# Optimization experiments

Measured on AMD Instinct MI355X. Metric: run time of the kernel, lower is better.

The kernel has to match this reference:

```python
import jax, jax.numpy as jnp
import numpy as np

DIM = 256
B, W_IN, H_IN = 8, 96, 96


def setup_inputs() -> dict:
    key = jax.random.key(0)
    k1, k2, k3 = jax.random.split(key, 3)
    x = jax.random.normal(k1, (B, W_IN, H_IN, DIM), dtype=jnp.float32)
    # Conv2d(dim, 3*dim, kernel_size=1): weight (3C, C) (1x1 spatial dropped), bias (3C,)
    w_qkv = jax.random.normal(k2, (3 * DIM, DIM), dtype=jnp.float32) * (1.0 / np.sqrt(DIM))
    b_qkv = jax.random.normal(k3, (3 * DIM,), dtype=jnp.float32) * 0.01
    return {"x": x, "w_qkv": w_qkv, "b_qkv": b_qkv}


def reference(x, w_qkv, b_qkv):
    # x: (B, W, H, C) -> transpose(3,1) -> (B, C, H, W)
    xt = jnp.transpose(x, (0, 3, 2, 1))
    # 1x1 conv == channel GEMM
    qvk = jnp.einsum('bchw,oc->bohw', xt, w_qkv) + b_qkv[None, :, None, None]
    q, k, v = jnp.split(qvk, 3, axis=1)  # each (B, C, H, W)
    Bn, C, H, W = q.shape

    q_t = jnp.transpose(q, (0, 2, 1, 3))            # (B, H, C, W)
    qk = q_t.reshape(Bn, H * C, W)                   # (B, H*C, W)
    qf = q_t.reshape(Bn, H, C * W)                   # (B, H, C*W)
    kq = jnp.transpose(k, (0, 1, 3, 2)).reshape(Bn, C * W, H)  # (B, C*W, H)
    ms = jax.nn.softmax(jnp.matmul(qf, kq), axis=-1)  # (B, H, H) attention over H

    kf = jnp.transpose(k, (0, 3, 2, 1)).reshape(Bn, W, H * C)  # (B, W, H*C)
    ma = jax.nn.softmax(jnp.matmul(kf, qk), axis=-1)  # (B, W, W) attention over W

    vq = jnp.transpose(v, (0, 2, 1, 3)).reshape(Bn, H, C * W)  # (B, H, C*W)
    vk = jnp.transpose(v, (0, 3, 2, 1)).reshape(Bn, W, H * C)  # (B, W, H*C)

    ms = jnp.matmul(ms, vq).reshape(Bn, H, C, W)     # view(B, H, C, W)
    ms = jnp.transpose(ms, (0, 2, 1, 3))             # (B, C, H, W)
    ma = jnp.matmul(ma, vk).reshape(Bn, W, H, C)     # view(B, W, H, C)
    ma = jnp.transpose(ma, (0, 3, 2, 1))             # (B, C, H, W)

    # final transpose(3,1): (B, C, H, W) -> (B, W, H, C)
    return jnp.transpose(ms + ma, (0, 3, 2, 1))
```

## Files before the change

kernel.cpp:

```cpp
#include <hip/hip_runtime.h>
#include <math.h>

#define SQ 96
#define CQ 256
#define OQ 768
#define HWQ 9216
#define PIXQ 73728

typedef __attribute__((ext_vector_type(8))) __bf16 bf16x8;
typedef __attribute__((ext_vector_type(4))) float f32x4;

union FragU { uint4 u; bf16x8 b; };

__device__ inline uint32_t bf16_rne_u(float f) {
  uint32_t u = __float_as_uint(f);
  return (u + 0x7FFFu + ((u >> 16) & 1u)) >> 16;
}
__device__ inline uint32_t pack_split(float f) {
  uint32_t hi = bf16_rne_u(f);
  float rem = f - __uint_as_float(hi << 16);
  uint32_t lo = __float_as_uint(rem) >> 16;
  return hi | (lo << 16);
}

__device__ inline const uint32_t* swzc(const uint32_t* base, int row, int colb) {
  return base + row * 32 + ((colb ^ ((row & 7) << 4)) >> 2);
}

__device__ inline void lds_dma16(const void* g, void* l) {
  __builtin_amdgcn_global_load_lds(
      (const __attribute__((address_space(1))) uint32_t*)g,
      (__attribute__((address_space(3))) uint32_t*)l, 16, 0, 0);
}

__global__ __launch_bounds__(256) void split_tiles_kernel(
    const float* __restrict__ src, uint32_t* __restrict__ dst) {
  int t = blockIdx.x * 256 + threadIdx.x;
  int e = t * 8;
  int m = e >> 8;
  int rem = e & 255;
  int kc = rem >> 5;
  int k8 = (rem & 31) >> 3;
  const float* s = src + (size_t)m * 256 + rem;
  uint32_t h[4], l[4];
#pragma unroll
  for (int i = 0; i < 2; ++i) {
    float4 v = *(const float4*)(s + 4 * i);
    uint32_t p0 = pack_split(v.x), p1 = pack_split(v.y);
    uint32_t p2 = pack_split(v.z), p3 = pack_split(v.w);
    h[2 * i]     = (p0 & 0xFFFFu) | (p1 << 16);
    h[2 * i + 1] = (p2 & 0xFFFFu) | (p3 << 16);
    l[2 * i]     = (p0 >> 16) | (p1 & 0xFFFF0000u);
    l[2 * i + 1] = (p2 >> 16) | (p3 & 0xFFFF0000u);
  }
  int swz = (m & 7) << 4;
  uint32_t* rowp = dst + ((size_t)m * 8 + kc) * 32;
  *(uint4*)(rowp + (((k8 * 16) ^ swz) >> 2)) = *(uint4*)h;
  *(uint4*)(rowp + (((64 + k8 * 16) ^ swz) >> 2)) = *(uint4*)l;
}

__global__ __launch_bounds__(256) void qkv_gemm_mfma(
    const uint32_t* __restrict__ xps, const uint32_t* __restrict__ wps,
    const float* __restrict__ bias, ushort* __restrict__ qkh,
    ushort* __restrict__ qkl, ushort* __restrict__ vb) {
  __shared__ uint32_t Apk[128 * 32];
  __shared__ uint32_t Bpk[128 * 32];
  const int tid = threadIdx.x;
  const int lane = tid & 63;
  const int wid = tid >> 6;
  const int wm = wid >> 1, wn = wid & 1;
  const int lr = lane & 15, quad = lane >> 4;
  const int lin = (blockIdx.x & 7) * 432 + (blockIdx.x >> 3);
  const int m0 = (lin / 6) * 128, n0 = (lin % 6) * 128;
  const int srow = tid >> 3;
  const int scol = (tid & 7) * 4;

  f32x4 acc[4][4] = {};

  const uint32_t* aP = xps + (size_t)(m0 + srow) * 256 + scol;
  const uint32_t* bP = wps + (size_t)(n0 + srow) * 256 + scol;

  for (int kc = 0; kc < 8; ++kc) {
#pragma unroll
    for (int j = 0; j < 4; ++j) {
      lds_dma16(aP + j * 8192 + kc * 32, &Apk[j * 1024 + tid * 4]);
      lds_dma16(bP + j * 8192 + kc * 32, &Bpk[j * 1024 + tid * 4]);
    }
    __syncthreads();

    FragU ah[4], al[4], bh[4], bl[4];
#pragma unroll
    for (int t = 0; t < 4; ++t) {
      const int ra = wm * 64 + t * 16 + lr;
      ah[t].u = *(const uint4*)swzc(Apk, ra, quad * 16);
      al[t].u = *(const uint4*)swzc(Apk, ra, 64 + quad * 16);
      const int rb = wn * 64 + t * 16 + lr;
      bh[t].u = *(const uint4*)swzc(Bpk, rb, quad * 16);
      bl[t].u = *(const uint4*)swzc(Bpk, rb, 64 + quad * 16);
    }
#pragma unroll
    for (int i = 0; i < 4; ++i)
#pragma unroll
      for (int j = 0; j < 4; ++j) {
        acc[i][j] = __builtin_amdgcn_mfma_f32_16x16x32_bf16(al[i].b, bh[j].b, acc[i][j], 0, 0, 0);
        acc[i][j] = __builtin_amdgcn_mfma_f32_16x16x32_bf16(ah[i].b, bl[j].b, acc[i][j], 0, 0, 0);
        acc[i][j] = __builtin_amdgcn_mfma_f32_16x16x32_bf16(ah[i].b, bh[j].b, acc[i][j], 0, 0, 0);
      }
    __syncthreads();
  }

#pragma unroll
  for (int i = 0; i < 4; ++i) {
    const int growb = m0 + wm * 64 + i * 16 + quad * 4;
#pragma unroll
    for (int r = 0; r < 4; ++r) {
      int p = growb + r;
      int b = p / HWQ;
      int rem = p - b * HWQ;
      int ww = rem / SQ;
      int hh = rem - ww * SQ;
      size_t opix = (size_t)b * HWQ + (size_t)hh * SQ + ww;
#pragma unroll
      for (int j = 0; j < 4; ++j) {
        int o = n0 + wn * 64 + j * 16 + lr;
        float val = acc[i][j][r] + bias[o];
        if (o < 512) {
          uint32_t ps = pack_split(val);
          qkh[opix * 512 + o] = (ushort)ps;
          qkl[opix * 512 + o] = (ushort)(ps >> 16);
        } else {
          vb[opix * 256 + (o - 512)] = (ushort)bf16_rne_u(val);
        }
      }
    }
  }
}

__global__ __launch_bounds__(256) void attn_scores_mfma(
    const ushort* __restrict__ qkh, const ushort* __restrict__ qkl,
    float* __restrict__ Sh, float* __restrict__ Sw) {
  __shared__ uint32_t Xpk[96 * 32];
  __shared__ uint32_t Ypk[96 * 32];
  const int tid = threadIdx.x;
  const int lane = tid & 63;
  const int wid = tid >> 6;
  const int wm = wid >> 1, wn = wid & 1;
  const int lr = lane & 15, quad = lane >> 4;
  const int chunk = blockIdx.x;
  const int b = blockIdx.y;
  const int which = blockIdx.z;
  const size_t base = (size_t)b * HWQ * 512;
  const int offX = which ? 256 : 0;
  const int offY = which ? 0 : 256;
  const int srow = tid >> 3;
  const int byteoff = (tid & 7) * 16;

  f32x4 acc[3][3] = {};

  for (int it = 0; it < 24; ++it) {
    int kout = chunk * 3 + (it >> 3);
    int c0 = (it & 7) * 32;
#pragma unroll
    for (int j = 0; j < 3; ++j) {
      int row = j * 32 + srow;
      int nom = byteoff ^ ((row & 7) << 4);
      const ushort* plane = (nom & 64) ? qkl : qkh;
      int within = (nom & 63) >> 1;
      size_t pix = which ? ((size_t)kout * SQ + row) : ((size_t)row * SQ + kout);
      const ushort* sX = plane + base + pix * 512 + offX + c0 + within;
      const ushort* sY = plane + base + pix * 512 + offY + c0 + within;
      lds_dma16(sX, &Xpk[j * 1024 + tid * 4]);
      lds_dma16(sY, &Ypk[j * 1024 + tid * 4]);
    }
    __syncthreads();

    FragU xh[3], xl[3], yh[3], yl[3];
#pragma unroll
    for (int t = 0; t < 3; ++t) {
      const int rx = wm * 48 + t * 16 + lr;
      xh[t].u = *(const uint4*)swzc(Xpk, rx, quad * 16);
      xl[t].u = *(const uint4*)swzc(Xpk, rx, 64 + quad * 16);
      const int ry = wn * 48 + t * 16 + lr;
      yh[t].u = *(const uint4*)swzc(Ypk, ry, quad * 16);
      yl[t].u = *(const uint4*)swzc(Ypk, ry, 64 + quad * 16);
    }
#pragma unroll
    for (int i = 0; i < 3; ++i)
#pragma unroll
      for (int j = 0; j < 3; ++j) {
        acc[i][j] = __builtin_amdgcn_mfma_f32_16x16x32_bf16(xl[i].b, yh[j].b, acc[i][j], 0, 0, 0);
        acc[i][j] = __builtin_amdgcn_mfma_f32_16x16x32_bf16(xh[i].b, yl[j].b, acc[i][j], 0, 0, 0);
        acc[i][j] = __builtin_amdgcn_mfma_f32_16x16x32_bf16(xh[i].b, yh[j].b, acc[i][j], 0, 0, 0);
      }
    __syncthreads();
  }
  float* S = which ? Sw : Sh;
#pragma unroll
  for (int i = 0; i < 3; ++i)
#pragma unroll
    for (int r = 0; r < 4; ++r)
#pragma unroll
      for (int j = 0; j < 3; ++j) {
        int row = wm * 48 + i * 16 + quad * 4 + r;
        int col = wn * 48 + j * 16 + lr;
        atomicAdd(S + ((size_t)b * SQ + row) * SQ + col, acc[i][j][r]);
      }
}

__global__ __launch_bounds__(256) void softmax_p(
    const float* __restrict__ Sh, const float* __restrict__ Sw,
    ushort* __restrict__ Pms, ushort* __restrict__ Pma) {
  const int tid = threadIdx.x;
  const int lane = tid & 63;
  const int row = blockIdx.x * 4 + (tid >> 6);
  const float* p = (row < 768) ? (Sh + (size_t)row * SQ)
                               : (Sw + (size_t)(row - 768) * SQ);
  ushort* q = (row < 768) ? (Pms + (size_t)row * SQ)
                          : (Pma + (size_t)(row - 768) * SQ);
  float v0 = p[lane];
  float v1 = (lane < 32) ? p[64 + lane] : -3.0e38f;
  float m = fmaxf(v0, v1);
#pragma unroll
  for (int off = 32; off > 0; off >>= 1) m = fmaxf(m, __shfl_xor(m, off));
  float e0 = __expf(v0 - m);
  float e1 = (lane < 32) ? __expf(v1 - m) : 0.0f;
  float s = e0 + e1;
#pragma unroll
  for (int off = 32; off > 0; off >>= 1) s += __shfl_xor(s, off);
  float inv = 1.0f / s;
  q[lane] = (ushort)bf16_rne_u(e0 * inv);
  if (lane < 32) q[64 + lane] = (ushort)bf16_rne_u(e1 * inv);
}

__global__ __launch_bounds__(256) void attn_apply_mfma(
    const ushort* __restrict__ vb, const ushort* __restrict__ P,
    float* __restrict__ out, const int which) {
  __shared__ ushort Vt[256 * 40];
  const int tid = threadIdx.x;
  const int lane = tid & 63;
  const int wid = tid >> 6;
  const int wm = wid >> 1, wn = wid & 1;
  const int lr = lane & 15, quad = lane >> 4;
  const int xi = blockIdx.x;
  const int b = blockIdx.y;

  f32x4 acc[3][8] = {};

  for (int k0 = 0; k0 < 96; k0 += 32) {
#pragma unroll
    for (int j = 0; j < 8; ++j) {
      int bi = j * 256 + tid;
      int c2 = bi & 127;
      int k2 = bi >> 7;
      int k = k0 + k2 * 2;
      int c = c2 * 2;
      size_t r0, r1;
      if (which == 0) {
        r0 = ((size_t)b * HWQ + (size_t)k * SQ + xi) * CQ + c;
        r1 = r0 + (size_t)SQ * CQ;
      } else {
        r0 = ((size_t)b * HWQ + (size_t)xi * SQ + k) * CQ + c;
        r1 = r0 + CQ;
      }
      uint32_t a0 = *(const uint32_t*)(vb + r0);
      uint32_t a1 = *(const uint32_t*)(vb + r1);
      uint32_t w0 = (a0 & 0xFFFFu) | (a1 << 16);
      uint32_t w1 = (a0 >> 16) | (a1 & 0xFFFF0000u);
      *(uint32_t*)&Vt[c * 40 + k2 * 2] = w0;
      *(uint32_t*)&Vt[(c + 1) * 40 + k2 * 2] = w1;
    }
    __syncthreads();
    FragU a[3];
#pragma unroll
    for (int t = 0; t < 3; ++t) {
      int row = wm * 48 + t * 16 + lr;
      const ushort* ps = P + ((size_t)b * SQ + row) * SQ + k0 + quad * 8;
      a[t].u = *(const uint4*)ps;
    }
#pragma unroll
    for (int j = 0; j < 8; ++j) {
      int cb = wn * 128 + j * 16 + lr;
      FragU bf;
      bf.u = *(const uint4*)&Vt[cb * 40 + quad * 8];
#pragma unroll
      for (int i = 0; i < 3; ++i)
        acc[i][j] = __builtin_amdgcn_mfma_f32_16x16x32_bf16(a[i].b, bf.b, acc[i][j], 0, 0, 0);
    }
    __syncthreads();
  }

#pragma unroll
  for (int i = 0; i < 3; ++i) {
#pragma unroll
    for (int r = 0; r < 4; ++r) {
      int mrow = wm * 48 + i * 16 + quad * 4 + r;
      size_t obase;
      if (which == 0) obase = (((size_t)b * SQ + xi) * SQ + mrow) * CQ;
      else            obase = (((size_t)b * SQ + mrow) * SQ + xi) * CQ;
#pragma unroll
      for (int j = 0; j < 8; ++j) {
        int c = wn * 128 + j * 16 + lr;
        if (which == 0) out[obase + c] = acc[i][j][r];
        else            out[obase + c] += acc[i][j][r];
      }
    }
  }
}

extern "C" void kernel_launch(void* const* d_in, const int* in_sizes, int n_in,
                              void* d_out, int out_size, void* d_ws,
                              size_t ws_size, hipStream_t stream) {
  const float* x = (const float*)d_in[0];
  const float* w = (const float*)d_in[1];
  const float* bias = (const float*)d_in[2];
  float* out = (float*)d_out;

  ushort* qkh = (ushort*)d_ws;
  ushort* qkl = qkh + (size_t)PIXQ * 512;
  ushort* vb  = qkl + (size_t)PIXQ * 512;
  float*  Sh  = (float*)(vb + (size_t)PIXQ * 256);
  float*  Sw  = Sh + PIXQ;
  ushort* Pms = (ushort*)(Sw + PIXQ);
  ushort* Pma = Pms + PIXQ;
  uint32_t* wps = (uint32_t*)(Pma + PIXQ);

  uint32_t* xps = (uint32_t*)d_out;

  hipMemsetAsync(Sh, 0, 2 * (size_t)PIXQ * sizeof(float), stream);

  split_tiles_kernel<<<dim3(9216), 256, 0, stream>>>(x, xps);
  split_tiles_kernel<<<dim3(96), 256, 0, stream>>>(w, wps);
  qkv_gemm_mfma<<<dim3(3456), 256, 0, stream>>>(xps, wps, bias, qkh, qkl, vb);
  attn_scores_mfma<<<dim3(32, 8, 2), 256, 0, stream>>>(qkh, qkl, Sh, Sw);
  softmax_p<<<dim3(384), 256, 0, stream>>>(Sh, Sw, Pms, Pma);
  attn_apply_mfma<<<dim3(96, 8), 256, 0, stream>>>(vb, Pms, out, 0);
  attn_apply_mfma<<<dim3(96, 8), 256, 0, stream>>>(vb, Pma, out, 1);
}
```

Before: 418.6 us.

## Double-buffer LDS in GEMM kernels and replace score atomics with partial-sum reduction

Adds double-buffered LDS staging to the QKV GEMM and the attention score kernels, so the next K-chunk's async loads are issued before the current chunk's MFMAs run. The score kernel stops doing atomicAdd into a zeroed buffer and instead writes per-chunk partial score tiles into the output buffer, which is now reused as scratch. The softmax kernel sums the 32 partials before normalising, which also removes the memset. The cost is doubled LDS per block, which may lower occupancy, plus extra global traffic for the partial tiles.

```diff
diff --git a/kernel.cpp b/kernel.cpp
--- a/kernel.cpp
+++ b/kernel.cpp
@@ -63,8 +63,8 @@
     const uint32_t* __restrict__ xps, const uint32_t* __restrict__ wps,
     const float* __restrict__ bias, ushort* __restrict__ qkh,
     ushort* __restrict__ qkl, ushort* __restrict__ vb) {
-  __shared__ uint32_t Apk[128 * 32];
-  __shared__ uint32_t Bpk[128 * 32];
+  __shared__ uint32_t Apk[2][128 * 32];
+  __shared__ uint32_t Bpk[2][128 * 32];
   const int tid = threadIdx.x;
   const int lane = tid & 63;
   const int wid = tid >> 6;
@@ -75,28 +75,35 @@
   const int srow = tid >> 3;
   const int scol = (tid & 7) * 4;
 
-  f32x4 acc[4][4] = {};
-
   const uint32_t* aP = xps + (size_t)(m0 + srow) * 256 + scol;
   const uint32_t* bP = wps + (size_t)(n0 + srow) * 256 + scol;
 
+  auto stage = [&](int buf, int kc) {
+#pragma unroll
+    for (int j = 0; j < 4; ++j) {
+      lds_dma16(aP + j * 8192 + kc * 32, &Apk[buf][j * 1024 + tid * 4]);
+      lds_dma16(bP + j * 8192 + kc * 32, &Bpk[buf][j * 1024 + tid * 4]);
+    }
+  };
+
+  f32x4 acc[4][4] = {};
+
+  stage(0, 0);
+  __syncthreads();
+
+  int cur = 0;
   for (int kc = 0; kc < 8; ++kc) {
-#pragma unroll
-    for (int j = 0; j < 4; ++j) {
-      lds_dma16(aP + j * 8192 + kc * 32, &Apk[j * 1024 + tid * 4]);
-      lds_dma16(bP + j * 8192 + kc * 32, &Bpk[j * 1024 + tid * 4]);
-    }
-    __syncthreads();
+    if (kc < 7) stage(cur ^ 1, kc + 1);
 
     FragU ah[4], al[4], bh[4], bl[4];
 #pragma unroll
     for (int t = 0; t < 4; ++t) {
       const int ra = wm * 64 + t * 16 + lr;
-      ah[t].u = *(const uint4*)swzc(Apk, ra, quad * 16);
-      al[t].u = *(const uint4*)swzc(Apk, ra, 64 + quad * 16);
+      ah[t].u = *(const uint4*)swzc(Apk[cur], ra, quad * 16);
+      al[t].u = *(const uint4*)swzc(Apk[cur], ra, 64 + quad * 16);
       const int rb = wn * 64 + t * 16 + lr;
-      bh[t].u = *(const uint4*)swzc(Bpk, rb, quad * 16);
-      bl[t].u = *(const uint4*)swzc(Bpk, rb, 64 + quad * 16);
+      bh[t].u = *(const uint4*)swzc(Bpk[cur], rb, quad * 16);
+      bl[t].u = *(const uint4*)swzc(Bpk[cur], rb, 64 + quad * 16);
     }
 #pragma unroll
     for (int i = 0; i < 4; ++i)
@@ -107,6 +114,7 @@
         acc[i][j] = __builtin_amdgcn_mfma_f32_16x16x32_bf16(ah[i].b, bh[j].b, acc[i][j], 0, 0, 0);
       }
     __syncthreads();
+    cur ^= 1;
   }
 
 #pragma unroll
@@ -138,9 +146,9 @@
 
 __global__ __launch_bounds__(256) void attn_scores_mfma(
     const ushort* __restrict__ qkh, const ushort* __restrict__ qkl,
-    float* __restrict__ Sh, float* __restrict__ Sw) {
-  __shared__ uint32_t Xpk[96 * 32];
-  __shared__ uint32_t Ypk[96 * 32];
+    float* __restrict__ Sp) {
+  __shared__ uint32_t Xpk[2][96 * 32];
+  __shared__ uint32_t Ypk[2][96 * 32];
   const int tid = threadIdx.x;
   const int lane = tid & 63;
   const int wid = tid >> 6;
@@ -155,9 +163,7 @@
   const int srow = tid >> 3;
   const int byteoff = (tid & 7) * 16;
 
-  f32x4 acc[3][3] = {};
-
-  for (int it = 0; it < 24; ++it) {
+  auto stage = [&](int buf, int it) {
     int kout = chunk * 3 + (it >> 3);
     int c0 = (it & 7) * 32;
 #pragma unroll
@@ -169,20 +175,29 @@
       size_t pix = which ? ((size_t)kout * SQ + row) : ((size_t)row * SQ + kout);
       const ushort* sX = plane + base + pix * 512 + offX + c0 + within;
       const ushort* sY = plane + base + pix * 512 + offY + c0 + within;
-      lds_dma16(sX, &Xpk[j * 1024 + tid * 4]);
-      lds_dma16(sY, &Ypk[j * 1024 + tid * 4]);
-    }
-    __syncthreads();
+      lds_dma16(sX, &Xpk[buf][j * 1024 + tid * 4]);
+      lds_dma16(sY, &Ypk[buf][j * 1024 + tid * 4]);
+    }
+  };
+
+  f32x4 acc[3][3] = {};
+
+  stage(0, 0);
+  __syncthreads();
+
+  int cur = 0;
+  for (int it = 0; it < 24; ++it) {
+    if (it < 23) stage(cur ^ 1, it + 1);
 
     FragU xh[3], xl[3], yh[3], yl[3];
 #pragma unroll
     for (int t = 0; t < 3; ++t) {
       const int rx = wm * 48 + t * 16 + lr;
-      xh[t].u = *(const uint4*)swzc(Xpk, rx, quad * 16);
-      xl[t].u = *(const uint4*)swzc(Xpk, rx, 64 + quad * 16);
+      xh[t].u = *(const uint4*)swzc(Xpk[cur], rx, quad * 16);
+      xl[t].u = *(const uint4*)swzc(Xpk[cur], rx, 64 + quad * 16);
       const int ry = wn * 48 + t * 16 + lr;
-      yh[t].u = *(const uint4*)swzc(Ypk, ry, quad * 16);
-      yl[t].u = *(const uint4*)swzc(Ypk, ry, 64 + quad * 16);
+      yh[t].u = *(const uint4*)swzc(Ypk[cur], ry, quad * 16);
+      yl[t].u = *(const uint4*)swzc(Ypk[cur], ry, 64 + quad * 16);
     }
 #pragma unroll
     for (int i = 0; i < 3; ++i)
@@ -193,8 +208,10 @@
         acc[i][j] = __builtin_amdgcn_mfma_f32_16x16x32_bf16(xh[i].b, yh[j].b, acc[i][j], 0, 0, 0);
       }
     __syncthreads();
-  }
-  float* S = which ? Sw : Sh;
+    cur ^= 1;
+  }
+
+  float* S = Sp + (((size_t)(which * 8 + b) * 32 + chunk)) * (size_t)HWQ;
 #pragma unroll
   for (int i = 0; i < 3; ++i)
 #pragma unroll
@@ -203,22 +220,32 @@
       for (int j = 0; j < 3; ++j) {
         int row = wm * 48 + i * 16 + quad * 4 + r;
         int col = wn * 48 + j * 16 + lr;
-        atomicAdd(S + ((size_t)b * SQ + row) * SQ + col, acc[i][j][r]);
+        S[(size_t)row * SQ + col] = acc[i][j][r];
       }
 }
 
 __global__ __launch_bounds__(256) void softmax_p(
-    const float* __restrict__ Sh, const float* __restrict__ Sw,
-    ushort* __restrict__ Pms, ushort* __restrict__ Pma) {
+    const float* __restrict__ Sp, ushort* __restrict__ Pms,
+    ushort* __restrict__ Pma) {
   const int tid = threadIdx.x;
   const int lane = tid & 63;
   const int row = blockIdx.x * 4 + (tid >> 6);
-  const float* p = (row < 768) ? (Sh + (size_t)row * SQ)
-                               : (Sw + (size_t)(row - 768) * SQ);
+  const int wsel = row >= 768;
+  const int rr = row - wsel * 768;
+  const int b = rr / SQ;
+  const int hr = rr - b * SQ;
+  const float* base = Sp + ((size_t)(wsel * 8 + b) * 32) * (size_t)HWQ
+                      + (size_t)hr * SQ;
+  float v0 = 0.0f, s1 = 0.0f;
+#pragma unroll 4
+  for (int ch = 0; ch < 32; ++ch) {
+    const float* p = base + (size_t)ch * HWQ;
+    v0 += p[lane];
+    if (lane < 32) s1 += p[64 + lane];
+  }
   ushort* q = (row < 768) ? (Pms + (size_t)row * SQ)
                           : (Pma + (size_t)(row - 768) * SQ);
-  float v0 = p[lane];
-  float v1 = (lane < 32) ? p[64 + lane] : -3.0e38f;
+  float v1 = (lane < 32) ? s1 : -3.0e38f;
   float m = fmaxf(v0, v1);
 #pragma unroll
   for (int off = 32; off > 0; off >>= 1) m = fmaxf(m, __shfl_xor(m, off));
@@ -318,21 +345,18 @@
   ushort* qkh = (ushort*)d_ws;
   ushort* qkl = qkh + (size_t)PIXQ * 512;
   ushort* vb  = qkl + (size_t)PIXQ * 512;
-  float*  Sh  = (float*)(vb + (size_t)PIXQ * 256);
-  float*  Sw  = Sh + PIXQ;
-  ushort* Pms = (ushort*)(Sw + PIXQ);
+  ushort* Pms = vb + (size_t)PIXQ * 256;
   ushort* Pma = Pms + PIXQ;
   uint32_t* wps = (uint32_t*)(Pma + PIXQ);
 
   uint32_t* xps = (uint32_t*)d_out;
-
-  hipMemsetAsync(Sh, 0, 2 * (size_t)PIXQ * sizeof(float), stream);
+  float* Sp = (float*)d_out;
 
   split_tiles_kernel<<<dim3(9216), 256, 0, stream>>>(x, xps);
   split_tiles_kernel<<<dim3(96), 256, 0, stream>>>(w, wps);
   qkv_gemm_mfma<<<dim3(3456), 256, 0, stream>>>(xps, wps, bias, qkh, qkl, vb);
-  attn_scores_mfma<<<dim3(32, 8, 2), 256, 0, stream>>>(qkh, qkl, Sh, Sw);
-  softmax_p<<<dim3(384), 256, 0, stream>>>(Sh, Sw, Pms, Pma);
+  attn_scores_mfma<<<dim3(32, 8, 2), 256, 0, stream>>>(qkh, qkl, Sp);
+  softmax_p<<<dim3(384), 256, 0, stream>>>(Sp, Pms, Pma);
   attn_apply_mfma<<<dim3(96, 8), 256, 0, stream>>>(vb, Pms, out, 0);
   attn_apply_mfma<<<dim3(96, 8), 256, 0, stream>>>(vb, Pma, out, 1);
 }
```

Result: slower. 428.2 us (+2.3%).

## Fold Wq^T·Wk into a precomputed matrix so the projection GEMM shrinks

Applied to the files above, without the earlier changes.

The Q and K weights are folded algebraically into a single 256x256 matrix G = Wq^T Wk. The projection GEMM now computes only y = x·G and V (N=512 instead of 768), and scores are formed directly from x and y. Bias cross-terms are computed separately as per-row and per-column correction vectors, accumulated in the x-split pass and added before the softmax. Score partials are written per chunk and summed in the softmax kernel instead of using atomics and a memset. In exchange this adds several small prep kernels, a larger partial-score buffer that the softmax must read, and a different rounding path through G.

```diff
diff --git a/kernel.cpp b/kernel.cpp
--- a/kernel.cpp
+++ b/kernel.cpp
@@ -3,7 +3,6 @@
 
 #define SQ 96
 #define CQ 256
-#define OQ 768
 #define HWQ 9216
 #define PIXQ 73728
 
@@ -33,36 +32,104 @@
       (__attribute__((address_space(3))) uint32_t*)l, 16, 0, 0);
 }
 
-__global__ __launch_bounds__(256) void split_tiles_kernel(
-    const float* __restrict__ src, uint32_t* __restrict__ dst) {
+__device__ inline void pack8_store(float4 va, float4 vb_, int m, int kc,
+                                   int k8, uint32_t* __restrict__ dst) {
+  uint32_t p0 = pack_split(va.x), p1 = pack_split(va.y);
+  uint32_t p2 = pack_split(va.z), p3 = pack_split(va.w);
+  uint32_t p4 = pack_split(vb_.x), p5 = pack_split(vb_.y);
+  uint32_t p6 = pack_split(vb_.z), p7 = pack_split(vb_.w);
+  uint32_t h[4], l[4];
+  h[0] = (p0 & 0xFFFFu) | (p1 << 16);
+  h[1] = (p2 & 0xFFFFu) | (p3 << 16);
+  h[2] = (p4 & 0xFFFFu) | (p5 << 16);
+  h[3] = (p6 & 0xFFFFu) | (p7 << 16);
+  l[0] = (p0 >> 16) | (p1 & 0xFFFF0000u);
+  l[1] = (p2 >> 16) | (p3 & 0xFFFF0000u);
+  l[2] = (p4 >> 16) | (p5 & 0xFFFF0000u);
+  l[3] = (p6 >> 16) | (p7 & 0xFFFF0000u);
+  int swz = (m & 7) << 4;
+  uint32_t* rowp = dst + ((size_t)m * 8 + kc) * 32;
+  *(uint4*)(rowp + (((k8 * 16) ^ swz) >> 2)) = *(uint4*)h;
+  *(uint4*)(rowp + (((64 + k8 * 16) ^ swz) >> 2)) = *(uint4*)l;
+}
+
+__global__ __launch_bounds__(256) void gemm_g_kernel(
+    const float* __restrict__ w, float* __restrict__ Gf) {
+  const int cp = blockIdx.x;
+  const int c = threadIdx.x;
+  float acc = 0.0f;
+#pragma unroll 4
+  for (int o = 0; o < 256; ++o)
+    acc += w[o * 256 + c] * w[(256 + o) * 256 + cp];
+  Gf[c * 256 + cp] = acc;
+}
+
+__global__ __launch_bounds__(256) void prep_vec_kernel(
+    const float* __restrict__ w, const float* __restrict__ bias,
+    float* __restrict__ tvec, float* __restrict__ svec) {
+  const int c = threadIdx.x;
+  float t = 0.0f, s = 0.0f;
+#pragma unroll 4
+  for (int o = 0; o < 256; ++o) {
+    t += bias[o] * w[(256 + o) * 256 + c];
+    s += bias[256 + o] * w[o * 256 + c];
+  }
+  tvec[c] = t;
+  svec[c] = s;
+}
+
+__global__ __launch_bounds__(256) void pack_b_kernel(
+    const float* __restrict__ Gf, const float* __restrict__ w,
+    uint32_t* __restrict__ Bps) {
   int t = blockIdx.x * 256 + threadIdx.x;
   int e = t * 8;
   int m = e >> 8;
   int rem = e & 255;
-  int kc = rem >> 5;
-  int k8 = (rem & 31) >> 3;
-  const float* s = src + (size_t)m * 256 + rem;
-  uint32_t h[4], l[4];
-#pragma unroll
-  for (int i = 0; i < 2; ++i) {
-    float4 v = *(const float4*)(s + 4 * i);
-    uint32_t p0 = pack_split(v.x), p1 = pack_split(v.y);
-    uint32_t p2 = pack_split(v.z), p3 = pack_split(v.w);
-    h[2 * i]     = (p0 & 0xFFFFu) | (p1 << 16);
-    h[2 * i + 1] = (p2 & 0xFFFFu) | (p3 << 16);
-    l[2 * i]     = (p0 >> 16) | (p1 & 0xFFFF0000u);
-    l[2 * i + 1] = (p2 >> 16) | (p3 & 0xFFFF0000u);
-  }
-  int swz = (m & 7) << 4;
-  uint32_t* rowp = dst + ((size_t)m * 8 + kc) * 32;
-  *(uint4*)(rowp + (((k8 * 16) ^ swz) >> 2)) = *(uint4*)h;
-  *(uint4*)(rowp + (((64 + k8 * 16) ^ swz) >> 2)) = *(uint4*)l;
+  const float* s = (m < 256) ? (Gf + (size_t)m * 256 + rem)
+                             : (w + (size_t)(m + 256) * 256 + rem);
+  float4 va = *(const float4*)s;
+  float4 vb_ = *(const float4*)(s + 4);
+  pack8_store(va, vb_, m, rem >> 5, (rem & 31) >> 3, Bps);
+}
+
+__global__ __launch_bounds__(256) void split_x_kernel(
+    const float* __restrict__ x, const float* __restrict__ tvec,
+    const float* __restrict__ svec, uint32_t* __restrict__ xps,
+    float* __restrict__ alpha, float* __restrict__ gamma) {
+  int t = blockIdx.x * 256 + threadIdx.x;
+  int e = t * 8;
+  int m = e >> 8;
+  int rem = e & 255;
+  const float* s = x + (size_t)m * 256 + rem;
+  float4 va = *(const float4*)s;
+  float4 vb_ = *(const float4*)(s + 4);
+  pack8_store(va, vb_, m, rem >> 5, (rem & 31) >> 3, xps);
+
+  const float* tv = tvec + rem;
+  const float* sv = svec + rem;
+  float td = va.x * tv[0] + va.y * tv[1] + va.z * tv[2] + va.w * tv[3]
+           + vb_.x * tv[4] + vb_.y * tv[5] + vb_.z * tv[6] + vb_.w * tv[7];
+  float sd = va.x * sv[0] + va.y * sv[1] + va.z * sv[2] + va.w * sv[3]
+           + vb_.x * sv[4] + vb_.y * sv[5] + vb_.z * sv[6] + vb_.w * sv[7];
+#pragma unroll
+  for (int off = 16; off > 0; off >>= 1) {
+    td += __shfl_xor(td, off);
+    sd += __shfl_xor(sd, off);
+  }
+  if ((threadIdx.x & 31) == 0) {
+    int b = m / HWQ;
+    int r = m - b * HWQ;
+    int ww = r / SQ;
+    int hh = r - ww * SQ;
+    atomicAdd(alpha + b * SQ + hh, td);
+    atomicAdd(gamma + b * SQ + ww, sd);
+  }
 }
 
 __global__ __launch_bounds__(256) void qkv_gemm_mfma(
-    const uint32_t* __restrict__ xps, const uint32_t* __restrict__ wps,
-    const float* __restrict__ bias, ushort* __restrict__ qkh,
-    ushort* __restrict__ qkl, ushort* __restrict__ vb) {
+    const uint32_t* __restrict__ xps, const uint32_t* __restrict__ Bps,
+    const float* __restrict__ bias, ushort* __restrict__ yps,
+    ushort* __restrict__ vb) {
   __shared__ uint32_t Apk[128 * 32];
   __shared__ uint32_t Bpk[128 * 32];
   const int tid = threadIdx.x;
@@ -70,15 +137,15 @@
   const int wid = tid >> 6;
   const int wm = wid >> 1, wn = wid & 1;
   const int lr = lane & 15, quad = lane >> 4;
-  const int lin = (blockIdx.x & 7) * 432 + (blockIdx.x >> 3);
-  const int m0 = (lin / 6) * 128, n0 = (lin % 6) * 128;
+  const int lin = (blockIdx.x & 7) * 288 + (blockIdx.x >> 3);
+  const int m0 = (lin >> 2) * 128, n0 = (lin & 3) * 128;
   const int srow = tid >> 3;
   const int scol = (tid & 7) * 4;
 
+  const uint32_t* aP = xps + (size_t)(m0 + srow) * 256 + scol;
+  const uint32_t* bP = Bps + (size_t)(n0 + srow) * 256 + scol;
+
   f32x4 acc[4][4] = {};
-
-  const uint32_t* aP = xps + (size_t)(m0 + srow) * 256 + scol;
-  const uint32_t* bP = wps + (size_t)(n0 + srow) * 256 + scol;
 
   for (int kc = 0; kc < 8; ++kc) {
 #pragma unroll
@@ -109,36 +176,52 @@
     __syncthreads();
   }
 
-#pragma unroll
-  for (int i = 0; i < 4; ++i) {
-    const int growb = m0 + wm * 64 + i * 16 + quad * 4;
-#pragma unroll
-    for (int r = 0; r < 4; ++r) {
-      int p = growb + r;
-      int b = p / HWQ;
-      int rem = p - b * HWQ;
-      int ww = rem / SQ;
-      int hh = rem - ww * SQ;
-      size_t opix = (size_t)b * HWQ + (size_t)hh * SQ + ww;
-#pragma unroll
-      for (int j = 0; j < 4; ++j) {
-        int o = n0 + wn * 64 + j * 16 + lr;
-        float val = acc[i][j][r] + bias[o];
-        if (o < 512) {
-          uint32_t ps = pack_split(val);
-          qkh[opix * 512 + o] = (ushort)ps;
-          qkl[opix * 512 + o] = (ushort)(ps >> 16);
-        } else {
-          vb[opix * 256 + (o - 512)] = (ushort)bf16_rne_u(val);
+  if (n0 < 256) {
+#pragma unroll
+    for (int i = 0; i < 4; ++i) {
+      const int growb = m0 + wm * 64 + i * 16 + quad * 4;
+#pragma unroll
+      for (int r = 0; r < 4; ++r) {
+        int p = growb + r;
+        size_t b16 = (size_t)p * 512;
+        int sw = (p & 7) << 4;
+#pragma unroll
+        for (int j = 0; j < 4; ++j) {
+          int o = n0 + wn * 64 + j * 16 + lr;
+          int ci = o & 31, kc = o >> 5;
+          uint32_t ps = pack_split(acc[i][j][r]);
+          size_t rb = b16 + (size_t)kc * 64;
+          yps[rb + (((ci * 2) ^ sw) >> 1)] = (ushort)ps;
+          yps[rb + (((64 + ci * 2) ^ sw) >> 1)] = (ushort)(ps >> 16);
         }
       }
     }
+  } else {
+#pragma unroll
+    for (int i = 0; i < 4; ++i) {
+      const int growb = m0 + wm * 64 + i * 16 + quad * 4;
+#pragma unroll
+      for (int r = 0; r < 4; ++r) {
+        int p = growb + r;
+        int b = p / HWQ;
+        int rem = p - b * HWQ;
+        int ww = rem / SQ;
+        int hh = rem - ww * SQ;
+        size_t opix = (size_t)b * HWQ + (size_t)hh * SQ + ww;
+#pragma unroll
+        for (int j = 0; j < 4; ++j) {
+          int o = n0 + wn * 64 + j * 16 + lr;
+          float val = acc[i][j][r] + bias[256 + o];
+          vb[opix * 256 + (o - 256)] = (ushort)bf16_rne_u(val);
+        }
+      }
+    }
   }
 }
 
 __global__ __launch_bounds__(256) void attn_scores_mfma(
-    const ushort* __restrict__ qkh, const ushort* __restrict__ qkl,
-    float* __restrict__ Sh, float* __restrict__ Sw) {
+    const ushort* __restrict__ xf, const ushort* __restrict__ yf,
+    float* __restrict__ Sp) {
   __shared__ uint32_t Xpk[96 * 32];
   __shared__ uint32_t Ypk[96 * 32];
   const int tid = threadIdx.x;
@@ -149,9 +232,8 @@
   const int chunk = blockIdx.x;
   const int b = blockIdx.y;
   const int which = blockIdx.z;
-  const size_t base = (size_t)b * HWQ * 512;
-  const int offX = which ? 256 : 0;
-  const int offY = which ? 0 : 256;
+  const ushort* Xf = which ? yf : xf;
+  const ushort* Yf = which ? xf : yf;
   const int srow = tid >> 3;
   const int byteoff = (tid & 7) * 16;
 
@@ -159,18 +241,16 @@
 
   for (int it = 0; it < 24; ++it) {
     int kout = chunk * 3 + (it >> 3);
-    int c0 = (it & 7) * 32;
+    int kc = it & 7;
 #pragma unroll
     for (int j = 0; j < 3; ++j) {
       int row = j * 32 + srow;
-      int nom = byteoff ^ ((row & 7) << 4);
-      const ushort* plane = (nom & 64) ? qkl : qkh;
-      int within = (nom & 63) >> 1;
-      size_t pix = which ? ((size_t)kout * SQ + row) : ((size_t)row * SQ + kout);
-      const ushort* sX = plane + base + pix * 512 + offX + c0 + within;
-      const ushort* sY = plane + base + pix * 512 + offY + c0 + within;
-      lds_dma16(sX, &Xpk[j * 1024 + tid * 4]);
-      lds_dma16(sY, &Ypk[j * 1024 + tid * 4]);
+      int pm = which ? (row * SQ + kout) : (kout * SQ + row);
+      int pix = b * HWQ + pm;
+      int nom = byteoff ^ (((row & 7) ^ (pix & 7)) << 4);
+      size_t off = ((size_t)pix * 8 + kc) * 64 + (nom >> 1);
+      lds_dma16(Xf + off, &Xpk[j * 1024 + tid * 4]);
+      lds_dma16(Yf + off, &Ypk[j * 1024 + tid * 4]);
     }
     __syncthreads();
 
@@ -194,7 +274,7 @@
       }
     __syncthreads();
   }
-  float* S = which ? Sw : Sh;
+  float* S = Sp + ((size_t)(which * 8 + b) * 32 + chunk) * (size_t)HWQ;
 #pragma unroll
   for (int i = 0; i < 3; ++i)
 #pragma unroll
@@ -203,22 +283,34 @@
       for (int j = 0; j < 3; ++j) {
         int row = wm * 48 + i * 16 + quad * 4 + r;
         int col = wn * 48 + j * 16 + lr;
-        atomicAdd(S + ((size_t)b * SQ + row) * SQ + col, acc[i][j][r]);
+        S[(size_t)row * SQ + col] = acc[i][j][r];
       }
 }
 
 __global__ __launch_bounds__(256) void softmax_p(
-    const float* __restrict__ Sh, const float* __restrict__ Sw,
-    ushort* __restrict__ Pms, ushort* __restrict__ Pma) {
+    const float* __restrict__ Sp, const float* __restrict__ alpha,
+    const float* __restrict__ gamma, ushort* __restrict__ Pms,
+    ushort* __restrict__ Pma) {
   const int tid = threadIdx.x;
   const int lane = tid & 63;
   const int row = blockIdx.x * 4 + (tid >> 6);
-  const float* p = (row < 768) ? (Sh + (size_t)row * SQ)
-                               : (Sw + (size_t)(row - 768) * SQ);
-  ushort* q = (row < 768) ? (Pms + (size_t)row * SQ)
-                          : (Pma + (size_t)(row - 768) * SQ);
-  float v0 = p[lane];
-  float v1 = (lane < 32) ? p[64 + lane] : -3.0e38f;
+  const int wsel = row >= 768;
+  const int rr = row - wsel * 768;
+  const int b = rr / SQ;
+  const int hr = rr - b * SQ;
+  const float* base = Sp + ((size_t)(wsel * 8 + b) * 32) * (size_t)HWQ
+                      + (size_t)hr * SQ;
+  float v0 = 0.0f, s1 = 0.0f;
+#pragma unroll 4
+  for (int ch = 0; ch < 32; ++ch) {
+    const float* p = base + (size_t)ch * HWQ;
+    v0 += p[lane];
+    if (lane < 32) s1 += p[64 + lane];
+  }
+  const float* corr = (wsel ? gamma : alpha) + b * SQ;
+  v0 += corr[lane];
+  ushort* q = wsel ? (Pma + (size_t)rr * SQ) : (Pms + (size_t)rr * SQ);
+  float v1 = (lane < 32) ? (s1 + corr[64 + lane]) : -3.0e38f;
   float m = fmaxf(v0, v1);
 #pragma unroll
   for (int off = 32; off > 0; off >>= 1) m = fmaxf(m, __shfl_xor(m, off));
@@ -315,24 +407,29 @@
   const float* bias = (const float*)d_in[2];
   float* out = (float*)d_out;
 
-  ushort* qkh = (ushort*)d_ws;
-  ushort* qkl = qkh + (size_t)PIXQ * 512;
-  ushort* vb  = qkl + (size_t)PIXQ * 512;
-  float*  Sh  = (float*)(vb + (size_t)PIXQ * 256);
-  float*  Sw  = Sh + PIXQ;
-  ushort* Pms = (ushort*)(Sw + PIXQ);
+  ushort* yps = (ushort*)d_ws;
+  ushort* vb  = yps + (size_t)PIXQ * 512;
+  ushort* Pms = vb + (size_t)PIXQ * 256;
   ushort* Pma = Pms + PIXQ;
-  uint32_t* wps = (uint32_t*)(Pma + PIXQ);
+  float*  Sp  = (float*)(Pma + PIXQ);
+  uint32_t* Bps = (uint32_t*)(Sp + (size_t)2 * 8 * 32 * HWQ);
+  float* Gf   = (float*)(Bps + 512 * 256);
+  float* tvec = Gf + 65536;
+  float* svec = tvec + 256;
+  float* alpha = svec + 256;
+  float* gamma = alpha + 768;
 
   uint32_t* xps = (uint32_t*)d_out;
 
-  hipMemsetAsync(Sh, 0, 2 * (size_t)PIXQ * sizeof(float), stream);
-
-  split_tiles_kernel<<<dim3(9216), 256, 0, stream>>>(x, xps);
-  split_tiles_kernel<<<dim3(96), 256, 0, stream>>>(w, wps);
-  qkv_gemm_mfma<<<dim3(3456), 256, 0, stream>>>(xps, wps, bias, qkh, qkl, vb);
-  attn_scores_mfma<<<dim3(32, 8, 2), 256, 0, stream>>>(qkh, qkl, Sh, Sw);
-  softmax_p<<<dim3(384), 256, 0, stream>>>(Sh, Sw, Pms, Pma);
+  hipMemsetAsync(alpha, 0, 2 * 768 * sizeof(float), stream);
+
+  gemm_g_kernel<<<dim3(256), 256, 0, stream>>>(w, Gf);
+  prep_vec_kernel<<<dim3(1), 256, 0, stream>>>(w, bias, tvec, svec);
+  pack_b_kernel<<<dim3(64), 256, 0, stream>>>(Gf, w, Bps);
+  split_x_kernel<<<dim3(9216), 256, 0, stream>>>(x, tvec, svec, xps, alpha, gamma);
+  qkv_gemm_mfma<<<dim3(2304), 256, 0, stream>>>(xps, Bps, bias, yps, vb);
+  attn_scores_mfma<<<dim3(32, 8, 2), 256, 0, stream>>>((const ushort*)xps, yps, Sp);
+  softmax_p<<<dim3(384), 256, 0, stream>>>(Sp, alpha, gamma, Pms, Pma);
   attn_apply_mfma<<<dim3(96, 8), 256, 0, stream>>>(vb, Pms, out, 0);
   attn_apply_mfma<<<dim3(96, 8), 256, 0, stream>>>(vb, Pma, out, 1);
 }
```

New measurement: 471.8 us. 1.13x slower.
